# Kernel optimization log

Hardware: AMD Instinct MI355X
Metric: run time of the kernel (lower is better)

Reference implementation:

```python
import jax, jax.numpy as jnp
import numpy as np

H, W = 256, 256
S, S_IDX, END_BIAS = 48, 3, 10
E_IDX = S - END_BIAS          # 38
N_ITER = E_IDX - (S_IDX + 1)  # 34 sequential segments after the start segment
OUT_WIN = 10                  # outlier1d window length
OUT_THRESH = 2.0


def setup_inputs() -> dict:
    key = jax.random.key(0)
    # (x, y) event coordinates in [0, W) x [0, H); t/p/b columns are unused by the module.
    events = jax.random.uniform(key, (16, 960000, 2), jnp.float32, minval=0.0, maxval=256.0)
    return {"events": events}


def _blur(a):
    """5x5 uniform (0.04) blur, SAME padding; a: [B, S, D] -> [B, S, D]."""
    k = jnp.full((1, 1, 5, 5), 0.04, jnp.float32)
    return jax.lax.conv_general_dilated(a[:, None], k, (1, 1), [(2, 2), (2, 2)])[:, 0]


def _outlier_flags(m):
    """outlier1d(m[b, si:si+10], thresh=2)[0] for si in [S_IDX+1, E_IDX). m: [B,S] -> bool [B,N_ITER]."""
    widx = (jnp.arange(N_ITER)[:, None] + S_IDX + 1) + jnp.arange(OUT_WIN)[None, :]
    w = m[:, widx]                                   # [B, N_ITER, 10]
    med = jnp.median(w, axis=-1, keepdims=True)
    diff = jnp.abs(w - med)
    mad = jnp.median(diff, axis=-1)                  # [B, N_ITER]
    return 0.6745 * diff[..., 0] / mad > OUT_THRESH


def reference(events):
    B, N, _ = events.shape
    segmentLen = N // S            # static python int
    Nu = segmentLen * S
    x = events[:, :Nu, 0].astype(jnp.int32)   # [B, Nu]
    y = events[:, :Nu, 1].astype(jnp.int32)
    chunks = jnp.repeat(jnp.arange(S), segmentLen)   # segment id per event, [Nu]
    bidx = jnp.arange(B)[:, None]

    # per-batch x-t / y-t histograms via scatter-add
    alongX = jnp.zeros((B, S, W), jnp.float32).at[bidx, chunks[None, :], x].add(1.0)
    alongY = jnp.zeros((B, S, H), jnp.float32).at[bidx, chunks[None, :], y].add(1.0)

    def proc_axis(along, D):
        flat = along.reshape(B, -1)
        cv = (flat.mean(-1) + 3.0 * jnp.std(flat, axis=-1, ddof=1))[:, None, None]
        a = _blur(jnp.clip(along, 0.0, cv))
        m = jnp.einsum('bsd,d->bs', a, jnp.arange(D, dtype=jnp.float32)) / segmentLen
        start = m[:, S_IDX:S_IDX + 1]
        aligned = jnp.round(m - start - (D // 2 - start)).astype(jnp.int32)
        return m, aligned

    meanX, alignedX = proc_axis(alongX, W)
    meanY, alignedY = proc_axis(alongY, H)
    is_out = _outlier_flags(meanX) | _outlier_flags(meanY)   # [B, N_ITER]

    def per_batch(xb, yb, aX, aY, outb):
        xs = jnp.clip(xb - aX[chunks], 0, W - 1)
        ys = jnp.clip(yb - aY[chunks], 0, H - 1)
        idx_c = (xs + W * ys).reshape(S, segmentLen)
        idx_v = (xs // 2 + (W // 2) * (ys // 2)).reshape(S, segmentLen)
        container0 = jnp.zeros(W * H, jnp.int32).at[idx_c[S_IDX]].add(1)
        ver0 = jnp.zeros((W // 2) * (H // 2), bool).at[idx_v[S_IDX]].set(True)

        def step(carry, inp):
            container, ver, stopped = carry
            ic, iv, is_o = inp
            ver_new = ver.at[iv].set(True)
            cnt = jnp.sum(ver_new).astype(jnp.float32)
            new_info = jnp.sum(jnp.logical_xor(ver_new, ver)).astype(jnp.float32)
            brk = new_info / cnt < 0.1
            do = (~stopped) & (~is_o) & (~brk)
            stopped = stopped | ((~stopped) & (~is_o) & brk)
            container = jnp.where(do, container.at[ic].add(1), container)
            ver = jnp.where(do, ver_new, ver)
            return (container, ver, stopped), None

        (container, _, _), _ = jax.lax.scan(
            step, (container0, ver0, jnp.array(False)),
            (idx_c[S_IDX + 1:E_IDX], idx_v[S_IDX + 1:E_IDX], outb))
        c = container.astype(jnp.float32)
        cv = c.mean() + 3.0 * jnp.std(c, ddof=1)
        return jnp.clip(c, 0.0, cv) / cv

    containers = jax.vmap(per_batch)(x, y, alignedX, alignedY, is_out)  # [B, W*H]
    return containers.reshape(B, 1, H, W)
```

## Files before the change

### kernel.cpp

```cpp
#include <hip/hip_runtime.h>

#define NB 16
#define NEV 960000
#define NS 48
#define SEG 20000
#define S_IDX 3
#define E_IDX 38
#define N_ITER 34
#define ND 256
#define NCH 35

__device__ inline void centroid_pl(const float* __restrict__ along,
                                   float cv, int sI, int lane,
                                   float* mf_out, int* ai_out) {
    float vals[4][5];
    #pragma unroll
    for (int k = 0; k < 4; ++k) {
        int d = lane + 64 * k;
        #pragma unroll
        for (int ds = -2; ds <= 2; ++ds) {
            int ss = sI + ds;
            vals[k][ds + 2] = (ss >= 0 && ss < NS) ? along[ss * ND + d] : 0.0f;
        }
    }
    double acc = 0.0;
    #pragma unroll
    for (int k = 0; k < 4; ++k) {
        int d = lane + 64 * k;
        int lo = d - 2 < 0 ? 0 : d - 2;
        int hi = d + 2 > 255 ? 255 : d + 2;
        double Wd = 0.5 * (double)(lo + hi) * (double)(hi - lo + 1);
        double t = 0.0;
        #pragma unroll
        for (int ds = -2; ds <= 2; ++ds) {
            int ss = sI + ds;
            if (ss >= 0 && ss < NS) t += (double)fminf(vals[k][ds + 2], cv);
        }
        acc += t * Wd;
    }
    for (int off = 32; off; off >>= 1) acc += __shfl_down(acc, off);
    float mf = (float)(acc * 0.04 / (double)SEG);
    *mf_out = mf;
    *ai_out = (int)rintf(mf - 128.0f);
}

__device__ inline float cv_from_sums(const unsigned long long* __restrict__ cvsums,
                                     int b, int axis) {
    double ts  = 960000.0;
    double ts2 = (double)cvsums[b * 2 + axis];
    const double N = (double)(NS * ND);
    double mean = ts / N;
    double var  = (ts2 - ts * ts / N) / (N - 1.0);
    return (float)(mean + 3.0 * sqrt(var));
}

__global__ __launch_bounds__(256) void hist_kernel(const float* __restrict__ events,
                                                   float* __restrict__ alongX,
                                                   float* __restrict__ alongY,
                                                   unsigned* __restrict__ compact,
                                                   unsigned* __restrict__ container,
                                                   unsigned* __restrict__ masks,
                                                   unsigned long long* __restrict__ cvsums,
                                                   unsigned long long* __restrict__ sums) {
    __shared__ unsigned hx[4][ND], hy[4][ND];
    __shared__ unsigned long long qredX[4], qredY[4];
    int tid = threadIdx.x;
    int blk = blockIdx.x;
    int b = blk / NS, c = blk % NS;
    int wave = tid >> 6, lane = tid & 63;
    #pragma unroll
    for (int j = 0; j < 4; j++) { hx[j][tid] = 0; hy[j][tid] = 0; }
    {
        uint4 z = {0u, 0u, 0u, 0u};
        for (int i = blk * 256 + tid; i < 262144; i += NB * NS * 256)
            ((uint4*)container)[i] = z;
        for (int i = blk * 256 + tid; i < 71680; i += NB * NS * 256)
            ((uint4*)masks)[i] = z;
        if (blk == 0 && tid < NB * 2) cvsums[tid] = 0ull;
        if (blk == 1 && tid < NB * 2) sums[tid] = 0ull;
    }
    __syncthreads();
    size_t base = (size_t)b * NEV + (size_t)c * SEG;
    const float4* ev4 = (const float4*)(events + base * 2);
    bool wr = (c >= S_IDX && c < E_IDX);
    uint4* dst = wr ? (uint4*)(compact + ((size_t)b * NCH + (c - S_IDX)) * (SEG / 2)) : nullptr;
    unsigned* HX = hx[wave];
    unsigned* HY = hy[wave];
    for (int k = tid; k < SEG / 8; k += 256) {
        float4 v0 = ev4[k], v1 = ev4[2500 + k], v2 = ev4[5000 + k], v3 = ev4[7500 + k];
        int x0 = (int)v0.x, y0 = (int)v0.y, x1 = (int)v0.z, y1 = (int)v0.w;
        int x2 = (int)v1.x, y2 = (int)v1.y, x3 = (int)v1.z, y3 = (int)v1.w;
        int x4 = (int)v2.x, y4 = (int)v2.y, x5 = (int)v2.z, y5 = (int)v2.w;
        int x6 = (int)v3.x, y6 = (int)v3.y, x7 = (int)v3.z, y7 = (int)v3.w;
        x0 = x0 > 255 ? 255 : x0; y0 = y0 > 255 ? 255 : y0;
        x1 = x1 > 255 ? 255 : x1; y1 = y1 > 255 ? 255 : y1;
        x2 = x2 > 255 ? 255 : x2; y2 = y2 > 255 ? 255 : y2;
        x3 = x3 > 255 ? 255 : x3; y3 = y3 > 255 ? 255 : y3;
        x4 = x4 > 255 ? 255 : x4; y4 = y4 > 255 ? 255 : y4;
        x5 = x5 > 255 ? 255 : x5; y5 = y5 > 255 ? 255 : y5;
        x6 = x6 > 255 ? 255 : x6; y6 = y6 > 255 ? 255 : y6;
        x7 = x7 > 255 ? 255 : x7; y7 = y7 > 255 ? 255 : y7;
        atomicAdd(&HX[x0], 1u); atomicAdd(&HY[y0], 1u);
        atomicAdd(&HX[x1], 1u); atomicAdd(&HY[y1], 1u);
        atomicAdd(&HX[x2], 1u); atomicAdd(&HY[y2], 1u);
        atomicAdd(&HX[x3], 1u); atomicAdd(&HY[y3], 1u);
        atomicAdd(&HX[x4], 1u); atomicAdd(&HY[y4], 1u);
        atomicAdd(&HX[x5], 1u); atomicAdd(&HY[y5], 1u);
        atomicAdd(&HX[x6], 1u); atomicAdd(&HY[y6], 1u);
        atomicAdd(&HX[x7], 1u); atomicAdd(&HY[y7], 1u);
        if (wr) {
            uint4 p;
            p.x = (unsigned)(x0 | (y0 << 8)) | ((unsigned)(x1 | (y1 << 8)) << 16);
            p.y = (unsigned)(x2 | (y2 << 8)) | ((unsigned)(x3 | (y3 << 8)) << 16);
            p.z = (unsigned)(x4 | (y4 << 8)) | ((unsigned)(x5 | (y5 << 8)) << 16);
            p.w = (unsigned)(x6 | (y6 << 8)) | ((unsigned)(x7 | (y7 << 8)) << 16);
            dst[k] = p;
        }
    }
    __syncthreads();
    unsigned sx = hx[0][tid] + hx[1][tid] + hx[2][tid] + hx[3][tid];
    unsigned sy = hy[0][tid] + hy[1][tid] + hy[2][tid] + hy[3][tid];
    int o = (b * NS + c) * ND + tid;
    alongX[o] = (float)sx;
    alongY[o] = (float)sy;
    unsigned long long qx = (unsigned long long)sx * sx;
    unsigned long long qy = (unsigned long long)sy * sy;
    for (int off = 32; off; off >>= 1) { qx += __shfl_down(qx, off); qy += __shfl_down(qy, off); }
    if (lane == 0) { qredX[wave] = qx; qredY[wave] = qy; }
    __syncthreads();
    if (tid == 0) {
        atomicAdd(&cvsums[b * 2],     qredX[0] + qredX[1] + qredX[2] + qredX[3]);
        atomicAdd(&cvsums[b * 2 + 1], qredY[0] + qredY[1] + qredY[2] + qredY[3]);
    }
}

__global__ __launch_bounds__(256) void mask_kernel(const unsigned* __restrict__ compact,
                                                   const float* __restrict__ alongX,
                                                   const float* __restrict__ alongY,
                                                   const unsigned long long* __restrict__ cvsums,
                                                   unsigned* __restrict__ masks) {
    __shared__ unsigned sm[512];
    __shared__ int sal[2];
    int tid = threadIdx.x, blk = blockIdx.x;
    int hi = blk & 1;
    int tile = blk >> 1;
    int b = tile / NCH, ci = tile % NCH, si = S_IDX + ci;
    int wave = tid >> 6, lane = tid & 63;
    sm[tid] = 0; sm[tid + 256] = 0;
    if (wave < 2) {
        const float* along = (wave ? alongY : alongX) + (size_t)b * NS * ND;
        float cv = cv_from_sums(cvsums, b, wave);
        float mf; int ai;
        centroid_pl(along, cv, si, lane, &mf, &ai);
        if (lane == 0) sal[wave] = ai;
    }
    __syncthreads();
    int aX = sal[0], aY = sal[1];
    const uint4* cp = (const uint4*)(compact + ((size_t)b * NCH + ci) * (SEG / 2));
    for (int i = hi * 1250 + tid; i < (hi + 1) * 1250; i += 256) {
        uint4 w = cp[i];
        unsigned wsv[4] = {w.x, w.y, w.z, w.w};
        #pragma unroll
        for (int j = 0; j < 4; j++) {
            unsigned v = wsv[j];
            #pragma unroll
            for (int h = 0; h < 2; h++) {
                unsigned e = (h ? (v >> 16) : v) & 0xFFFFu;
                int xs = (int)(e & 255u) - aX; xs = xs < 0 ? 0 : (xs > 255 ? 255 : xs);
                int ys = (int)(e >> 8)   - aY; ys = ys < 0 ? 0 : (ys > 255 ? 255 : ys);
                int iv = (xs >> 1) | ((ys >> 1) << 7);
                atomicOr(&sm[iv >> 5], 1u << (iv & 31));
            }
        }
    }
    __syncthreads();
    unsigned* mo = masks + (size_t)tile * 512;
    unsigned v0 = sm[tid], v1 = sm[tid + 256];
    if (v0) atomicOr(&mo[tid], v0);
    if (v1) atomicOr(&mo[tid + 256], v1);
}

__device__ inline float median10(const float* v) {
    float w[10];
    #pragma unroll
    for (int i = 0; i < 10; i++) w[i] = v[i];
    #pragma unroll
    for (int i = 1; i < 10; i++) {
        float k = w[i]; int j = i - 1;
        while (j >= 0 && w[j] > k) { w[j + 1] = w[j]; j--; }
        w[j + 1] = k;
    }
    return 0.5f * (w[4] + w[5]);
}

__device__ inline bool outlier_flag(const float* w) {
    float med = median10(w);
    float d[10];
    #pragma unroll
    for (int i = 0; i < 10; i++) d[i] = fabsf(w[i] - med);
    float d0 = d[0];
    float mad = median10(d);
    return (0.6745f * d0 / mad) > 2.0f;
}

__device__ inline unsigned wave_sum_u32(unsigned v) {
    for (int off = 32; off; off >>= 1) v += __shfl_xor(v, off);
    return v;
}

__global__ __launch_bounds__(1024) void decide_kernel(const unsigned* __restrict__ masks,
                                                      const float* __restrict__ alongX,
                                                      const float* __restrict__ alongY,
                                                      const unsigned long long* __restrict__ cvsums,
                                                      int* __restrict__ alignedX,
                                                      int* __restrict__ alignedY,
                                                      unsigned long long* __restrict__ commitmask) {
    __shared__ float mlds[2 * NS];
    int b = blockIdx.x, tid = threadIdx.x;
    int wave = tid >> 6, lane = tid & 63;
    float cv0 = cv_from_sums(cvsums, b, 0);
    float cv1 = cv_from_sums(cvsums, b, 1);
    #pragma unroll
    for (int q = 0; q < 6; ++q) {
        int p = wave + 16 * q;
        int ax = p >= NS;
        int sI = p - NS * ax;
        const float* along = (ax ? alongY : alongX) + (size_t)b * NS * ND;
        float mf; int ai;
        centroid_pl(along, ax ? cv1 : cv0, sI, lane, &mf, &ai);
        if (lane == 0) {
            mlds[ax * NS + sI] = mf;
            (ax ? alignedY : alignedX)[b * NS + sI] = ai;
        }
    }
    __syncthreads();
    if (tid < 64) {
        const unsigned* mb = masks + (size_t)b * NCH * 512;
        uint4 v0 = ((const uint4*)mb)[lane * 2];
        uint4 v1 = ((const uint4*)mb)[lane * 2 + 1];
        const uint4* pp = (const uint4*)(mb + 512);
        uint4 p0 = pp[lane * 2], p1 = pp[lane * 2 + 1];
        bool f = false;
        if (lane < N_ITER) {
            const float* mx = &mlds[0];
            const float* my = &mlds[NS];
            f = outlier_flag(&mx[S_IDX + 1 + lane]) || outlier_flag(&my[S_IDX + 1 + lane]);
        }
        unsigned long long omask = __ballot(f);
        unsigned ver[8] = {v0.x, v0.y, v0.z, v0.w, v1.x, v1.y, v1.z, v1.w};
        unsigned pc = 0;
        #pragma unroll
        for (int j = 0; j < 8; j++) pc += __popc(ver[j]);
        unsigned cnt = wave_sum_u32(pc);
        unsigned long long cm = 1ull;
        for (int idx = 1; idx < NCH; ++idx) {
            uint4 c0 = p0, c1 = p1;
            if (idx + 1 < NCH) {
                const uint4* np = (const uint4*)(mb + (size_t)(idx + 1) * 512);
                p0 = np[lane * 2]; p1 = np[lane * 2 + 1];
            }
            unsigned del[8] = {c0.x, c0.y, c0.z, c0.w, c1.x, c1.y, c1.z, c1.w};
            unsigned nl = 0;
            #pragma unroll
            for (int j = 0; j < 8; j++) nl += __popc(del[j] & ~ver[j]);
            unsigned ni = wave_sum_u32(nl);
            bool is_o = (omask >> (idx - 1)) & 1;
            if (!is_o) {
                unsigned cn = cnt + ni;
                float ratio = (float)ni / (float)cn;
                if (ratio < 0.1f) break;
                cm |= 1ull << idx;
                cnt = cn;
                #pragma unroll
                for (int j = 0; j < 8; j++) ver[j] |= del[j];
            }
        }
        if (lane == 0) commitmask[b] = cm;
    }
}

__global__ __launch_bounds__(256) void commit_kernel(const unsigned* __restrict__ compact,
                                                     const int* __restrict__ alignedX,
                                                     const int* __restrict__ alignedY,
                                                     const unsigned long long* __restrict__ commitmask,
                                                     unsigned* __restrict__ container) {
    int blk = blockIdx.x, tid = threadIdx.x;
    int qi = blk & 3;
    int tile = blk >> 2;
    int b = tile / NCH, ci = tile % NCH;
    if (!((commitmask[b] >> ci) & 1ull)) return;
    int si = S_IDX + ci;
    int aX = alignedX[b * NS + si], aY = alignedY[b * NS + si];
    unsigned* cont = container + (size_t)b * 65536;
    const uint4* cp = (const uint4*)(compact + ((size_t)b * NCH + ci) * (SEG / 2));
    for (int i = qi * 625 + tid; i < (qi + 1) * 625; i += 256) {
        uint4 w = cp[i];
        unsigned wsv[4] = {w.x, w.y, w.z, w.w};
        #pragma unroll
        for (int j = 0; j < 4; j++) {
            unsigned v = wsv[j];
            #pragma unroll
            for (int h = 0; h < 2; h++) {
                unsigned e = (h ? (v >> 16) : v) & 0xFFFFu;
                int xs = (int)(e & 255u) - aX; xs = xs < 0 ? 0 : (xs > 255 ? 255 : xs);
                int ys = (int)(e >> 8)   - aY; ys = ys < 0 ? 0 : (ys > 255 ? 255 : ys);
                atomicAdd(&cont[xs | (ys << 8)], 1u);
            }
        }
    }
}

__global__ __launch_bounds__(256) void cv_kernel(const unsigned* __restrict__ container,
                                                 unsigned long long* __restrict__ sums) {
    __shared__ unsigned long long sredA[4], sredB[4];
    int tid = threadIdx.x, blk = blockIdx.x;
    int b = blk >> 4, part = blk & 15;
    const uint4* c4 = (const uint4*)(container + (size_t)b * 65536) + part * 1024;
    unsigned long long s = 0, s2 = 0;
    for (int i = tid; i < 1024; i += 256) {
        uint4 v = c4[i];
        s  += (unsigned long long)v.x + v.y + v.z + v.w;
        s2 += (unsigned long long)v.x * v.x + (unsigned long long)v.y * v.y
            + (unsigned long long)v.z * v.z + (unsigned long long)v.w * v.w;
    }
    for (int off = 32; off; off >>= 1) { s += __shfl_down(s, off); s2 += __shfl_down(s2, off); }
    if ((tid & 63) == 0) { sredA[tid >> 6] = s; sredB[tid >> 6] = s2; }
    __syncthreads();
    if (tid == 0) {
        atomicAdd(&sums[b * 2],     sredA[0] + sredA[1] + sredA[2] + sredA[3]);
        atomicAdd(&sums[b * 2 + 1], sredB[0] + sredB[1] + sredB[2] + sredB[3]);
    }
}

__global__ __launch_bounds__(256) void finish_kernel(const unsigned* __restrict__ container,
                                                     const unsigned long long* __restrict__ sums,
                                                     float* __restrict__ out) {
    int g = blockIdx.x * 256 + threadIdx.x;
    int b = g >> 14;
    double ts  = (double)sums[b * 2];
    double ts2 = (double)sums[b * 2 + 1];
    double mean = ts / 65536.0;
    double var  = (ts2 - ts * ts / 65536.0) / 65535.0;
    float cv = (float)(mean + 3.0 * sqrt(var));
    uint4 v = ((const uint4*)container)[g];
    float4 o;
    o.x = fminf((float)v.x, cv) / cv;
    o.y = fminf((float)v.y, cv) / cv;
    o.z = fminf((float)v.z, cv) / cv;
    o.w = fminf((float)v.w, cv) / cv;
    ((float4*)out)[g] = o;
}

extern "C" void kernel_launch(void* const* d_in, const int* in_sizes, int n_in,
                              void* d_out, int out_size, void* d_ws, size_t ws_size,
                              hipStream_t stream) {
    const float* events = (const float*)d_in[0];
    float* out = (float*)d_out;
    char* ws = (char*)d_ws;

    float*    alongX    = (float*)(ws);
    float*    alongY    = (float*)(ws + 786432);
    unsigned* container = (unsigned*)(ws + 1572864);
    int*      alignedX  = (int*)(ws + 5767168);
    int*      alignedY  = (int*)(ws + 5770240);
    unsigned long long* commitmask = (unsigned long long*)(ws + 5779456);
    unsigned long long* sums       = (unsigned long long*)(ws + 5779584);
    unsigned long long* cvsums     = (unsigned long long*)(ws + 5779840);
    unsigned* compact   = (unsigned*)(ws + 6291456);
    unsigned* masks     = (unsigned*)(ws + 29360128);

    hist_kernel<<<NB * NS, 256, 0, stream>>>(events, alongX, alongY, compact,
                                             container, masks, cvsums, sums);
    mask_kernel<<<NB * NCH * 2, 256, 0, stream>>>(compact, alongX, alongY, cvsums, masks);
    decide_kernel<<<NB, 1024, 0, stream>>>(masks, alongX, alongY, cvsums,
                                           alignedX, alignedY, commitmask);
    commit_kernel<<<NB * NCH * 4, 256, 0, stream>>>(compact, alignedX, alignedY,
                                                    commitmask, container);
    cv_kernel<<<NB * 16, 256, 0, stream>>>(container, sums);
    finish_kernel<<<1024, 256, 0, stream>>>(container, sums, out);
}
```

Measured before the change: 268.7 us.

## Remove decide kernel; fold centroids into mask kernel and replicate decision walk

The single-wave-per-batch decide_kernel launch is removed. Per-segment centroids and alignments are now computed by the otherwise idle waves of mask_kernel and written to a shared m_all buffer. Each commit_kernel block redoes the outlier and break decision walk itself before scattering its events. This cuts a kernel launch and a serial, low-occupancy stage. In exchange, every commit block repeats the 35-step mask walk, adding redundant L2 traffic and latency at the start of each block.

```diff
diff --git a/kernel.cpp b/kernel.cpp
--- a/kernel.cpp
+++ b/kernel.cpp
@@ -52,6 +52,79 @@
     double mean = ts / N;
     double var  = (ts2 - ts * ts / N) / (N - 1.0);
     return (float)(mean + 3.0 * sqrt(var));
+}
+
+__device__ inline float median10(const float* v) {
+    float w[10];
+    #pragma unroll
+    for (int i = 0; i < 10; i++) w[i] = v[i];
+    #pragma unroll
+    for (int i = 1; i < 10; i++) {
+        float k = w[i]; int j = i - 1;
+        while (j >= 0 && w[j] > k) { w[j + 1] = w[j]; j--; }
+        w[j + 1] = k;
+    }
+    return 0.5f * (w[4] + w[5]);
+}
+
+__device__ inline bool outlier_flag(const float* w) {
+    float med = median10(w);
+    float d[10];
+    #pragma unroll
+    for (int i = 0; i < 10; i++) d[i] = fabsf(w[i] - med);
+    float d0 = d[0];
+    float mad = median10(d);
+    return (0.6745f * d0 / mad) > 2.0f;
+}
+
+__device__ inline unsigned wave_sum_u32(unsigned v) {
+    for (int off = 32; off; off >>= 1) v += __shfl_xor(v, off);
+    return v;
+}
+
+__device__ inline unsigned long long decision_walk(const unsigned* __restrict__ mb,
+                                                   const float* __restrict__ m_b,
+                                                   int lane) {
+    uint4 v0 = ((const uint4*)mb)[lane * 2];
+    uint4 v1 = ((const uint4*)mb)[lane * 2 + 1];
+    const uint4* pp = (const uint4*)(mb + 512);
+    uint4 p0 = pp[lane * 2], p1 = pp[lane * 2 + 1];
+    bool f = false;
+    if (lane < N_ITER) {
+        const float* mx = m_b;
+        const float* my = m_b + NS;
+        f = outlier_flag(&mx[S_IDX + 1 + lane]) || outlier_flag(&my[S_IDX + 1 + lane]);
+    }
+    unsigned long long omask = __ballot(f);
+    unsigned ver[8] = {v0.x, v0.y, v0.z, v0.w, v1.x, v1.y, v1.z, v1.w};
+    unsigned pc = 0;
+    #pragma unroll
+    for (int j = 0; j < 8; j++) pc += __popc(ver[j]);
+    unsigned cnt = wave_sum_u32(pc);
+    unsigned long long cm = 1ull;
+    for (int idx = 1; idx < NCH; ++idx) {
+        uint4 c0 = p0, c1 = p1;
+        if (idx + 1 < NCH) {
+            const uint4* np = (const uint4*)(mb + (size_t)(idx + 1) * 512);
+            p0 = np[lane * 2]; p1 = np[lane * 2 + 1];
+        }
+        unsigned del[8] = {c0.x, c0.y, c0.z, c0.w, c1.x, c1.y, c1.z, c1.w};
+        unsigned nl = 0;
+        #pragma unroll
+        for (int j = 0; j < 8; j++) nl += __popc(del[j] & ~ver[j]);
+        unsigned ni = wave_sum_u32(nl);
+        bool is_o = (omask >> (idx - 1)) & 1;
+        if (!is_o) {
+            unsigned cn = cnt + ni;
+            float ratio = (float)ni / (float)cn;
+            if (ratio < 0.1f) break;
+            cm |= 1ull << idx;
+            cnt = cn;
+            #pragma unroll
+            for (int j = 0; j < 8; j++) ver[j] |= del[j];
+        }
+    }
+    return cm;
 }
 
 __global__ __launch_bounds__(256) void hist_kernel(const float* __restrict__ events,
@@ -138,7 +211,10 @@
                                                    const float* __restrict__ alongX,
                                                    const float* __restrict__ alongY,
                                                    const unsigned long long* __restrict__ cvsums,
-                                                   unsigned* __restrict__ masks) {
+                                                   unsigned* __restrict__ masks,
+                                                   float* __restrict__ m_all,
+                                                   int* __restrict__ alignedX,
+                                                   int* __restrict__ alignedY) {
     __shared__ unsigned sm[512];
     __shared__ int sal[2];
     int tid = threadIdx.x, blk = blockIdx.x;
@@ -152,7 +228,21 @@
         float cv = cv_from_sums(cvsums, b, wave);
         float mf; int ai;
         centroid_pl(along, cv, si, lane, &mf, &ai);
-        if (lane == 0) sal[wave] = ai;
+        if (lane == 0) {
+            sal[wave] = ai;
+            if (hi == 0) {
+                m_all[(b * 2 + wave) * NS + si] = mf;
+                (wave ? alignedY : alignedX)[b * NS + si] = ai;
+            }
+        }
+    } else if (hi == 1 && ci < 9) {
+        int ax = wave - 2;
+        int sx = E_IDX + ci;
+        const float* along = (ax ? alongY : alongX) + (size_t)b * NS * ND;
+        float cv = cv_from_sums(cvsums, b, ax);
+        float mf; int ai;
+        centroid_pl(along, cv, sx, lane, &mf, &ai);
+        if (lane == 0) m_all[(b * 2 + ax) * NS + sx] = mf;
     }
     __syncthreads();
     int aX = sal[0], aY = sal[1];
@@ -180,115 +270,24 @@
     if (v1) atomicOr(&mo[tid + 256], v1);
 }
 
-__device__ inline float median10(const float* v) {
-    float w[10];
-    #pragma unroll
-    for (int i = 0; i < 10; i++) w[i] = v[i];
-    #pragma unroll
-    for (int i = 1; i < 10; i++) {
-        float k = w[i]; int j = i - 1;
-        while (j >= 0 && w[j] > k) { w[j + 1] = w[j]; j--; }
-        w[j + 1] = k;
-    }
-    return 0.5f * (w[4] + w[5]);
-}
-
-__device__ inline bool outlier_flag(const float* w) {
-    float med = median10(w);
-    float d[10];
-    #pragma unroll
-    for (int i = 0; i < 10; i++) d[i] = fabsf(w[i] - med);
-    float d0 = d[0];
-    float mad = median10(d);
-    return (0.6745f * d0 / mad) > 2.0f;
-}
-
-__device__ inline unsigned wave_sum_u32(unsigned v) {
-    for (int off = 32; off; off >>= 1) v += __shfl_xor(v, off);
-    return v;
-}
-
-__global__ __launch_bounds__(1024) void decide_kernel(const unsigned* __restrict__ masks,
-                                                      const float* __restrict__ alongX,
-                                                      const float* __restrict__ alongY,
-                                                      const unsigned long long* __restrict__ cvsums,
-                                                      int* __restrict__ alignedX,
-                                                      int* __restrict__ alignedY,
-                                                      unsigned long long* __restrict__ commitmask) {
-    __shared__ float mlds[2 * NS];
-    int b = blockIdx.x, tid = threadIdx.x;
-    int wave = tid >> 6, lane = tid & 63;
-    float cv0 = cv_from_sums(cvsums, b, 0);
-    float cv1 = cv_from_sums(cvsums, b, 1);
-    #pragma unroll
-    for (int q = 0; q < 6; ++q) {
-        int p = wave + 16 * q;
-        int ax = p >= NS;
-        int sI = p - NS * ax;
-        const float* along = (ax ? alongY : alongX) + (size_t)b * NS * ND;
-        float mf; int ai;
-        centroid_pl(along, ax ? cv1 : cv0, sI, lane, &mf, &ai);
-        if (lane == 0) {
-            mlds[ax * NS + sI] = mf;
-            (ax ? alignedY : alignedX)[b * NS + sI] = ai;
-        }
-    }
-    __syncthreads();
-    if (tid < 64) {
-        const unsigned* mb = masks + (size_t)b * NCH * 512;
-        uint4 v0 = ((const uint4*)mb)[lane * 2];
-        uint4 v1 = ((const uint4*)mb)[lane * 2 + 1];
-        const uint4* pp = (const uint4*)(mb + 512);
-        uint4 p0 = pp[lane * 2], p1 = pp[lane * 2 + 1];
-        bool f = false;
-        if (lane < N_ITER) {
-            const float* mx = &mlds[0];
-            const float* my = &mlds[NS];
-            f = outlier_flag(&mx[S_IDX + 1 + lane]) || outlier_flag(&my[S_IDX + 1 + lane]);
-        }
-        unsigned long long omask = __ballot(f);
-        unsigned ver[8] = {v0.x, v0.y, v0.z, v0.w, v1.x, v1.y, v1.z, v1.w};
-        unsigned pc = 0;
-        #pragma unroll
-        for (int j = 0; j < 8; j++) pc += __popc(ver[j]);
-        unsigned cnt = wave_sum_u32(pc);
-        unsigned long long cm = 1ull;
-        for (int idx = 1; idx < NCH; ++idx) {
-            uint4 c0 = p0, c1 = p1;
-            if (idx + 1 < NCH) {
-                const uint4* np = (const uint4*)(mb + (size_t)(idx + 1) * 512);
-                p0 = np[lane * 2]; p1 = np[lane * 2 + 1];
-            }
-            unsigned del[8] = {c0.x, c0.y, c0.z, c0.w, c1.x, c1.y, c1.z, c1.w};
-            unsigned nl = 0;
-            #pragma unroll
-            for (int j = 0; j < 8; j++) nl += __popc(del[j] & ~ver[j]);
-            unsigned ni = wave_sum_u32(nl);
-            bool is_o = (omask >> (idx - 1)) & 1;
-            if (!is_o) {
-                unsigned cn = cnt + ni;
-                float ratio = (float)ni / (float)cn;
-                if (ratio < 0.1f) break;
-                cm |= 1ull << idx;
-                cnt = cn;
-                #pragma unroll
-                for (int j = 0; j < 8; j++) ver[j] |= del[j];
-            }
-        }
-        if (lane == 0) commitmask[b] = cm;
-    }
-}
-
 __global__ __launch_bounds__(256) void commit_kernel(const unsigned* __restrict__ compact,
                                                      const int* __restrict__ alignedX,
                                                      const int* __restrict__ alignedY,
-                                                     const unsigned long long* __restrict__ commitmask,
+                                                     const unsigned* __restrict__ masks,
+                                                     const float* __restrict__ m_all,
                                                      unsigned* __restrict__ container) {
+    __shared__ unsigned long long cm_sh;
     int blk = blockIdx.x, tid = threadIdx.x;
     int qi = blk & 3;
     int tile = blk >> 2;
     int b = tile / NCH, ci = tile % NCH;
-    if (!((commitmask[b] >> ci) & 1ull)) return;
+    if (tid < 64) {
+        unsigned long long cm = decision_walk(masks + (size_t)b * NCH * 512,
+                                              m_all + b * 2 * NS, tid);
+        if (tid == 0) cm_sh = cm;
+    }
+    __syncthreads();
+    if (!((cm_sh >> ci) & 1ull)) return;
     int si = S_IDX + ci;
     int aX = alignedX[b * NS + si], aY = alignedY[b * NS + si];
     unsigned* cont = container + (size_t)b * 65536;
@@ -363,7 +362,7 @@
     unsigned* container = (unsigned*)(ws + 1572864);
     int*      alignedX  = (int*)(ws + 5767168);
     int*      alignedY  = (int*)(ws + 5770240);
-    unsigned long long* commitmask = (unsigned long long*)(ws + 5779456);
+    float*    m_all     = (float*)(ws + 5773312);
     unsigned long long* sums       = (unsigned long long*)(ws + 5779584);
     unsigned long long* cvsums     = (unsigned long long*)(ws + 5779840);
     unsigned* compact   = (unsigned*)(ws + 6291456);
@@ -371,11 +370,10 @@
 
     hist_kernel<<<NB * NS, 256, 0, stream>>>(events, alongX, alongY, compact,
                                              container, masks, cvsums, sums);
-    mask_kernel<<<NB * NCH * 2, 256, 0, stream>>>(compact, alongX, alongY, cvsums, masks);
-    decide_kernel<<<NB, 1024, 0, stream>>>(masks, alongX, alongY, cvsums,
-                                           alignedX, alignedY, commitmask);
+    mask_kernel<<<NB * NCH * 2, 256, 0, stream>>>(compact, alongX, alongY, cvsums,
+                                                  masks, m_all, alignedX, alignedY);
     commit_kernel<<<NB * NCH * 4, 256, 0, stream>>>(compact, alignedX, alignedY,
-                                                    commitmask, container);
+                                                    masks, m_all, container);
     cv_kernel<<<NB * 16, 256, 0, stream>>>(container, sums);
     finish_kernel<<<1024, 256, 0, stream>>>(container, sums, out);
 }
```

After: 283.5 us. 1.06x slower.
